# Optimization experiments

Hardware: AMD Instinct MI355X
Metric: run time of the kernel (lower is better)

Reference implementation:

```python
import jax, jax.numpy as jnp
import numpy as np


def _bicubic_warp(img, dx, dy):
    """Faithful JAX port of Warp_Object.forward with flag='bicubic'.
    img: [B,C,H,W] float32; dx, dy: [B,1,H,W] pixel displacements.
    Replicates the original tile-order quirk: X/Y are repeated C times along
    dim0 (order c*B+b) while the image is flattened in b*C+c order.
    """
    B, C, H, W = img.shape
    Wm1 = jnp.float32(max(W - 1, 1))
    Hm1 = jnp.float32(max(H - 1, 1))
    xs = jnp.arange(W, dtype=jnp.float32)
    ys = jnp.arange(H, dtype=jnp.float32)
    Xg, Yg = jnp.meshgrid(xs, ys)          # [H,W]
    # normalized grid in [-1,1] as in forward()
    newX = 2.0 * (Xg[None] + dx[:, 0]) / Wm1 - 1.0   # [B,H,W]
    newY = 2.0 * (Yg[None] + dy[:, 0]) / Hm1 - 1.0
    # repeat over channels exactly like X.repeat([C,1,1,1]) (tile order)
    x_map = (jnp.tile(newX, (C, 1, 1)) + 1.0) * Wm1 / 2.0   # [B*C,H,W]
    y_map = (jnp.tile(newY, (C, 1, 1)) + 1.0) * Hm1 / 2.0

    x0 = jnp.floor(x_map)
    y0 = jnp.floor(y_map)
    tx = x_map - x0
    ty = y_map - y0

    def cubic_coeffs(t):
        cm1 = (-t ** 3 + 2.0 * t ** 2 - t) / 2.0
        c0 = (3.0 * t ** 3 - 5.0 * t ** 2 + 2.0) / 2.0
        c1 = (-3.0 * t ** 3 + 4.0 * t ** 2 + t) / 2.0
        c2 = 1.0 - (cm1 + c0 + c1)
        return (cm1, c0, c1, c2)

    cx = cubic_coeffs(tx)
    cy = cubic_coeffs(ty)

    x0i = x0.astype(jnp.int32)
    y0i = y0.astype(jnp.int32)
    xi = [jnp.clip(x0i + o, 0, W - 1) for o in (-1, 0, 1, 2)]
    yi = [jnp.clip(y0i + o, 0, H - 1) for o in (-1, 0, 1, 2)]

    flat = img.reshape(B * C, H, W)
    row = jnp.arange(B * C)[:, None, None]   # per-image base offset

    out = jnp.zeros_like(x_map)
    for j in range(4):            # 4 rows of the 4x4 bicubic stencil
        row_acc = jnp.zeros_like(x_map)
        for i in range(4):
            row_acc = row_acc + cx[i] * flat[row, yi[j], xi[i]]
        out = out + cy[j] * row_acc
    return out.reshape(B, C, H, W)


def setup_inputs() -> dict:
    key = jax.random.key(0)
    k1, k2, k3 = jax.random.split(key, 3)
    B, C, H, W = 4, 3, 512, 512
    input_image = jax.random.normal(k1, (B, C, H, W), dtype=jnp.float32)
    delta_x = jax.random.normal(k2, (B, 1, H, W), dtype=jnp.float32) * 1.5
    delta_y = jax.random.normal(k3, (B, 1, H, W), dtype=jnp.float32) * 1.5
    return {"input_image": input_image, "delta_x": delta_x, "delta_y": delta_y}


def reference(input_image, delta_x, delta_y):
    return _bicubic_warp(input_image, delta_x, delta_y)
```

## Files before the change

### kernel.cpp

```cpp
#include <hip/hip_runtime.h>


constexpr int B = 4, C = 3, H = 512, W = 512;
constexpr int HW = H * W;
constexpr int TH = 8;
constexpr int HALO_UP = 6, HALO_DN = 6;
constexpr int RS = TH + HALO_UP + HALO_DN;
constexpr int LST = 272;
constexpr int CH_ROW = LST / 4;
constexpr int NCHUNK = RS * CH_ROW;
constexpr int TILE_DW = RS * LST;
constexpr int NPOS = 2;
constexpr int NT = 1024;
constexpr int NB = B * (H / TH) * 2;

typedef float f4 __attribute__((ext_vector_type(4)));
typedef f4 f4u __attribute__((aligned(4)));

typedef const __attribute__((address_space(1))) void* gas_t;
typedef __attribute__((address_space(3))) void* las_t;

__device__ __forceinline__ void gload_lds16(const float* g, float* l) {
    __builtin_amdgcn_global_load_lds((gas_t)g, (las_t)l, 16, 0, 0);
}

__global__ __launch_bounds__(NT, 8)
void warp_bicubic_1bar(const float* __restrict__ img,
                       const float* __restrict__ dxp,
                       const float* __restrict__ dyp,
                       float* __restrict__ out)
{
    __shared__ float tile[C][TILE_DW];

    int b   = blockIdx.x;
    int swz = (b & 7) * (NB / 8) + (b >> 3);
    int bd   = swz >> 7;
    int band = (swz >> 1) & 63;
    int half = swz & 1;
    int yb   = band * TH;
    int xb   = half * 256;
    int cb   = half ? 248 : 0;

    int tid  = threadIdx.x;
    int wave = tid >> 6;
    int ry   = wave >> 1;
    int hw   = wave & 1;
    int lane = tid & 63;
    int y    = yb + ry;
    int xs   = xb + hw * 128 + lane;
    int pixoff = y * W + xs;

#pragma unroll
    for (int c = 0; c < C; ++c) {
        const float* plane = img + (size_t)(bd + 4 * c) * HW;
        for (int cc = tid; cc < NCHUNK; cc += NT) {
            int r  = cc / CH_ROW;
            int c4 = (cc - r * CH_ROW) * 4;
            int scol = min(cb + c4, W - 4);
            int sr   = min(max(yb - HALO_UP + r, 0), H - 1);
            gload_lds16(plane + sr * W + scol, &tile[c][cc * 4]);
        }
    }

    float dxa[NPOS], dya[NPOS];
#pragma unroll
    for (int p = 0; p < NPOS; ++p) {
        dxa[p] = __builtin_nontemporal_load(dxp + bd * HW + pixoff + 64 * p);
        dya[p] = __builtin_nontemporal_load(dyp + bd * HW + pixoff + 64 * p);
    }

    float wx[NPOS][4];
    float cyw[NPOS][4];
    int   lbase[NPOS];
    unsigned relv[NPOS], lsv[NPOS];
    bool  intile[NPOS];
#pragma unroll
    for (int p = 0; p < NPOS; ++p) {
        int x = xs + 64 * p;
        float xm = (float)x + dxa[p];
        float ym = (float)y + dya[p];
        float x0f = floorf(xm), y0f = floorf(ym);
        float tx = xm - x0f, ty = ym - y0f;
        int x0 = (int)x0f, y0 = (int)y0f;
        int s  = min(max(x0 - 1, 0), W - 4);

        float tx2 = tx * tx, tx3 = tx2 * tx;
        float cx0 = (-tx3 + 2.0f * tx2 - tx) * 0.5f;
        float cx1 = (3.0f * tx3 - 5.0f * tx2 + 2.0f) * 0.5f;
        float cx2 = (-3.0f * tx3 + 4.0f * tx2 + tx) * 0.5f;
        float cx3 = 1.0f - (cx0 + cx1 + cx2);

        float ty2 = ty * ty, ty3 = ty2 * ty;
        cyw[p][0] = (-ty3 + 2.0f * ty2 - ty) * 0.5f;
        cyw[p][1] = (3.0f * ty3 - 5.0f * ty2 + 2.0f) * 0.5f;
        cyw[p][2] = (-3.0f * ty3 + 4.0f * ty2 + ty) * 0.5f;
        cyw[p][3] = 1.0f - (cyw[p][0] + cyw[p][1] + cyw[p][2]);

        if (__builtin_expect(x0 >= 1 && x0 <= W - 3, 1)) {
            wx[p][0] = cx0; wx[p][1] = cx1; wx[p][2] = cx2; wx[p][3] = cx3;
        } else {
            float w0 = 0.f, w1 = 0.f, w2 = 0.f, w3 = 0.f;
            const float cxa[4] = {cx0, cx1, cx2, cx3};
#pragma unroll
            for (int o = 0; o < 4; ++o) {
                int xi = min(max(x0 - 1 + o, 0), W - 1);
                int e  = xi - s;
                float c = cxa[o];
                w0 += (e == 0) ? c : 0.f;
                w1 += (e == 1) ? c : 0.f;
                w2 += (e == 2) ? c : 0.f;
                w3 += (e == 3) ? c : 0.f;
            }
            wx[p][0] = w0; wx[p][1] = w1; wx[p][2] = w2; wx[p][3] = w3;
        }

        relv[p]  = (unsigned)(y0 - (yb - HALO_UP + 1));
        lsv[p]   = (unsigned)(s - cb);
        intile[p] = (relv[p] <= (unsigned)(RS - 4)) & (lsv[p] <= (unsigned)(LST - 4));
        lbase[p] = (int)relv[p] * LST + (int)lsv[p];
    }

    __syncthreads();

#pragma unroll
    for (int c = 0; c < C; ++c) {
        int kp = bd + 4 * c;
        const float* __restrict__ plane = img + (size_t)kp * HW;
        const float* __restrict__ tp = &tile[c][0];
        float* __restrict__ obase = out + (size_t)kp * HW + pixoff;
#pragma unroll
        for (int p = 0; p < NPOS; ++p) {
            float acc;
            if (__builtin_expect(intile[p], 1)) {
                const float* rp = tp + lbase[p];
                float r0 = cyw[p][0] * (wx[p][0]*rp[0] + wx[p][1]*rp[1] + wx[p][2]*rp[2] + wx[p][3]*rp[3]);
                rp += LST;
                float r1 = cyw[p][1] * (wx[p][0]*rp[0] + wx[p][1]*rp[1] + wx[p][2]*rp[2] + wx[p][3]*rp[3]);
                rp += LST;
                float r2 = cyw[p][2] * (wx[p][0]*rp[0] + wx[p][1]*rp[1] + wx[p][2]*rp[2] + wx[p][3]*rp[3]);
                rp += LST;
                float r3 = cyw[p][3] * (wx[p][0]*rp[0] + wx[p][1]*rp[1] + wx[p][2]*rp[2] + wx[p][3]*rp[3]);
                acc = (r0 + r1) + (r2 + r3);
            } else {
                int y0 = (int)relv[p] + (yb - HALO_UP + 1);
                int s  = (int)lsv[p] + cb;
                acc = 0.f;
#pragma unroll
                for (int j = 0; j < 4; ++j) {
                    int yi = min(max(y0 - 1 + j, 0), H - 1);
                    f4 v = *(const f4u*)(plane + yi * W + s);
                    acc += cyw[p][j] * (wx[p][0]*v.x + wx[p][1]*v.y + wx[p][2]*v.z + wx[p][3]*v.w);
                }
            }
            __builtin_nontemporal_store(acc, obase + 64 * p);
        }
    }
}

extern "C" void kernel_launch(void* const* d_in, const int* in_sizes, int n_in,
                              void* d_out, int out_size, void* d_ws, size_t ws_size,
                              hipStream_t stream) {
    const float* img = (const float*)d_in[0];
    const float* dx  = (const float*)d_in[1];
    const float* dy  = (const float*)d_in[2];
    float* out = (float*)d_out;

    dim3 block(NT);
    dim3 grid(NB);
    hipLaunchKernelGGL(warp_bicubic_1bar, grid, block, 0, stream,
                       img, dx, dy, out);
}
```

Before: 16.61 us.

## Pipeline per-channel LDS tile loads with staged vmcnt-gated barriers

The single barrier after loading all three channel tiles is replaced by a barrier before each channel's compute, gated by a partial `s_waitcnt vmcnt(4)`. Channel 0 interpolation can then start while the channel 1 and 2 tiles are still loading. Tile chunks are now assigned to fixed waves (two issues per wave per channel) instead of a strided loop. The dx/dy loads are issued before the tile loads. The fixed vmcnt(4) threshold ignores the output stores and fallback global loads issued between phases, so later channels may not be fully resident when read. That is a correctness risk, and two extra barriers are added.

```diff
diff --git a/kernel.cpp b/kernel.cpp
--- a/kernel.cpp
+++ b/kernel.cpp
@@ -9,6 +9,7 @@
 constexpr int LST = 272;
 constexpr int CH_ROW = LST / 4;
 constexpr int NCHUNK = RS * CH_ROW;
+constexpr int CPW = NCHUNK / 16;
 constexpr int TILE_DW = RS * LST;
 constexpr int NPOS = 2;
 constexpr int NT = 1024;
@@ -24,8 +25,15 @@
     __builtin_amdgcn_global_load_lds((gas_t)g, (las_t)l, 16, 0, 0);
 }
 
+#define PHASE_GATE() do {                                   \
+    asm volatile("s_waitcnt vmcnt(4)" ::: "memory");        \
+    __builtin_amdgcn_sched_barrier(0);                      \
+    __builtin_amdgcn_s_barrier();                           \
+    __builtin_amdgcn_sched_barrier(0);                      \
+} while (0)
+
 __global__ __launch_bounds__(NT, 8)
-void warp_bicubic_1bar(const float* __restrict__ img,
+void warp_bicubic_pipe(const float* __restrict__ img,
                        const float* __restrict__ dxp,
                        const float* __restrict__ dyp,
                        float* __restrict__ out)
@@ -42,31 +50,35 @@
     int cb   = half ? 248 : 0;
 
     int tid  = threadIdx.x;
-    int wave = tid >> 6;
-    int ry   = wave >> 1;
-    int hw   = wave & 1;
+    int wv   = tid >> 6;
     int lane = tid & 63;
+    int ry   = wv >> 1;
+    int hw   = wv & 1;
     int y    = yb + ry;
     int xs   = xb + hw * 128 + lane;
     int pixoff = y * W + xs;
-
-#pragma unroll
-    for (int c = 0; c < C; ++c) {
-        const float* plane = img + (size_t)(bd + 4 * c) * HW;
-        for (int cc = tid; cc < NCHUNK; cc += NT) {
-            int r  = cc / CH_ROW;
-            int c4 = (cc - r * CH_ROW) * 4;
-            int scol = min(cb + c4, W - 4);
-            int sr   = min(max(yb - HALO_UP + r, 0), H - 1);
-            gload_lds16(plane + sr * W + scol, &tile[c][cc * 4]);
-        }
-    }
 
     float dxa[NPOS], dya[NPOS];
 #pragma unroll
     for (int p = 0; p < NPOS; ++p) {
         dxa[p] = __builtin_nontemporal_load(dxp + bd * HW + pixoff + 64 * p);
         dya[p] = __builtin_nontemporal_load(dyp + bd * HW + pixoff + 64 * p);
+    }
+
+#pragma unroll
+    for (int c = 0; c < C; ++c) {
+        const float* plane = img + (size_t)(bd + 4 * c) * HW;
+#pragma unroll
+        for (int i = 0; i < 2; ++i) {
+            int chunk = wv * CPW + i * 64 + lane;
+            if (i == 0 || lane < CPW - 64) {
+                int r  = chunk / CH_ROW;
+                int c4 = (chunk - r * CH_ROW) * 4;
+                int scol = min(cb + c4, W - 4);
+                int sr   = min(max(yb - HALO_UP + r, 0), H - 1);
+                gload_lds16(plane + sr * W + scol, &tile[c][chunk * 4]);
+            }
+        }
     }
 
     float wx[NPOS][4];
@@ -120,10 +132,10 @@
         lbase[p] = (int)relv[p] * LST + (int)lsv[p];
     }
 
-    __syncthreads();
-
 #pragma unroll
     for (int c = 0; c < C; ++c) {
+        PHASE_GATE();
+
         int kp = bd + 4 * c;
         const float* __restrict__ plane = img + (size_t)kp * HW;
         const float* __restrict__ tp = &tile[c][0];
@@ -167,6 +179,6 @@
 
     dim3 block(NT);
     dim3 grid(NB);
-    hipLaunchKernelGGL(warp_bicubic_1bar, grid, block, 0, stream,
+    hipLaunchKernelGGL(warp_bicubic_pipe, grid, block, 0, stream,
                        img, dx, dy, out);
 }
```

Result: no change. 16.88 us (+1.6%).
